# Kernel tuning notes

Hardware: AMD Instinct MI355X
Metric: run time of the kernel (lower is better)

## Reference

```python
import jax, jax.numpy as jnp
import numpy as np

SEQ_LEN = 2048
EMB_DIM = 1024
HIDDEN = 1024
VOCAB = 50257
OUT = 50257


def setup_inputs() -> dict:
    key = jax.random.key(0)
    ks = jax.random.split(key, 8)
    s = 0.02
    input_seq = jax.random.randint(ks[0], (SEQ_LEN,), 0, VOCAB)
    emb = jax.random.normal(ks[1], (VOCAB, EMB_DIM), dtype=jnp.float32) * s
    # PyTorch nn.LSTM params: weight_ih [4H, E], weight_hh [4H, H], biases [4H]
    W_ih = jax.random.normal(ks[2], (4 * HIDDEN, EMB_DIM), dtype=jnp.float32) * s
    W_hh = jax.random.normal(ks[3], (4 * HIDDEN, HIDDEN), dtype=jnp.float32) * s
    b_ih = jax.random.normal(ks[4], (4 * HIDDEN,), dtype=jnp.float32) * s
    b_hh = jax.random.normal(ks[5], (4 * HIDDEN,), dtype=jnp.float32) * s
    W_out = jax.random.normal(ks[6], (OUT, HIDDEN), dtype=jnp.float32) * s
    b_out = jax.random.normal(ks[7], (OUT,), dtype=jnp.float32) * s
    return {"input_seq": input_seq, "emb": emb, "W_ih": W_ih, "W_hh": W_hh,
            "b_ih": b_ih, "b_hh": b_hh, "W_out": W_out, "b_out": b_out}


def _lstm_forward(x, W_ih, W_hh, b_ih, b_hh):
    # x: [S, E]; batch dim (=1 in the torch module) is collapsed away.
    H = W_hh.shape[1]
    # Precompute input contribution to all gates for every timestep: [S, 4H]
    x_gates = x @ W_ih.T + (b_ih + b_hh)

    def step(carry, xg):
        h, c = carry
        g = xg + h @ W_hh.T  # [4H]
        i, f, gg, o = jnp.split(g, 4)  # PyTorch gate order: i, f, g, o
        i = jax.nn.sigmoid(i)
        f = jax.nn.sigmoid(f)
        gg = jnp.tanh(gg)
        o = jax.nn.sigmoid(o)
        c = f * c + i * gg
        h = o * jnp.tanh(c)
        return (h, c), h

    h0 = jnp.zeros((H,), dtype=x.dtype)
    c0 = jnp.zeros((H,), dtype=x.dtype)
    _, hs = jax.lax.scan(step, (h0, c0), x_gates)
    return hs  # [S, H]


def reference(input_seq, emb, W_ih, W_hh, b_ih, b_hh, W_out, b_out):
    x = emb[input_seq]  # [S, E] embedding lookup
    hs = _lstm_forward(x, W_ih, W_hh, b_ih, b_hh)  # [S, H]
    logits = hs @ W_out.T + b_out  # [S, OUT]
    return jax.nn.log_softmax(logits, axis=1)
```

## Files before the change

kernel.cpp:

```cpp
#include <hip/hip_runtime.h>
#include <hip/hip_bf16.h>

#define SEQ 2048
#define EMB 1024
#define HID 1024
#define G4  4096
#define VOC 50257
#define VPAD 50304
#define KDIM 1024

typedef short bhalf8 __attribute__((ext_vector_type(8)));
typedef float f32x4  __attribute__((ext_vector_type(4)));

typedef __attribute__((address_space(3))) void lds_void;
typedef __attribute__((address_space(1))) const void gbl_cvoid;

__device__ __forceinline__ void direct_lds16(void* lds, const void* g) {
    __builtin_amdgcn_global_load_lds((gbl_cvoid*)g, (lds_void*)lds, 16, 0, 0);
}

__device__ __forceinline__ unsigned short f2b(float f) {
    unsigned u = __float_as_uint(f);
    unsigned r = u + 0x7fffu + ((u >> 16) & 1u);
    return (unsigned short)(r >> 16);
}

__global__ void f32_to_bf16_k(const float* __restrict__ src, unsigned short* __restrict__ dst,
                              long n_src, long n_dst) {
    long i = ((long)blockIdx.x * 256 + threadIdx.x) * 4;
    if (i >= n_dst) return;
    unsigned short o0 = 0, o1 = 0, o2 = 0, o3 = 0;
    if (i < n_src) {
        f32x4 v = *(const f32x4*)&src[i];
        o0 = f2b(v[0]); o1 = f2b(v[1]); o2 = f2b(v[2]); o3 = f2b(v[3]);
    }
    ushort4 o; o.x = o0; o.y = o1; o.z = o2; o.w = o3;
    *(ushort4*)&dst[i] = o;
}

__global__ void embed_cvt_k(const int* __restrict__ seq, const float* __restrict__ emb,
                            unsigned short* __restrict__ xb) {
    int s = blockIdx.x;
    int k = threadIdx.x * 4;
    long row = (long)seq[s] * EMB;
    f32x4 v = *(const f32x4*)&emb[row + k];
    ushort4 o; o.x = f2b(v[0]); o.y = f2b(v[1]); o.z = f2b(v[2]); o.w = f2b(v[3]);
    *(ushort4*)&xb[(long)s * EMB + k] = o;
}

__global__ void bias_sum_k(const float* __restrict__ a, const float* __restrict__ b,
                           float* __restrict__ o) {
    int i = blockIdx.x * 256 + threadIdx.x;
    if (i < G4) o[i] = a[i] + b[i];
}

__global__ __launch_bounds__(256)
void gemm_bt_k(const unsigned short* __restrict__ A, const unsigned short* __restrict__ Bt,
               const float* __restrict__ bias, float* __restrict__ C,
               int M, int Nreal, int K, int ldc) {
    __shared__ unsigned short lA[128 * 64];
    __shared__ unsigned short lB[128 * 64];
    const int tid  = threadIdx.x;
    const int wave = tid >> 6;
    const int lane = tid & 63;
    const int m0 = blockIdx.x * 128;
    const int n0 = blockIdx.y * 128;
    const int wm = (wave >> 1) * 64;
    const int wn = (wave & 1) * 64;
    const int quad = lane >> 4, l16 = lane & 15;
    const int srow = lane >> 3;
    const int scol = (lane & 7) * 8;

    f32x4 acc[4][4] = {};

    for (int k0 = 0; k0 < K; k0 += 64) {
#pragma unroll
        for (int c = 0; c < 4; ++c) {
            int r0 = wave * 32 + c * 8;
            const unsigned short* ga = A  + (long)(m0 + r0 + srow) * K + k0 + scol;
            direct_lds16(&lA[r0 * 64], ga);
            const unsigned short* gb = Bt + (long)(n0 + r0 + srow) * K + k0 + scol;
            direct_lds16(&lB[r0 * 64], gb);
        }
        __syncthreads();
#pragma unroll
        for (int kk = 0; kk < 2; ++kk) {
            bhalf8 af[4], bf[4];
#pragma unroll
            for (int i = 0; i < 4; ++i) {
                af[i] = *(const bhalf8*)&lA[(wm + i * 16 + l16) * 64 + kk * 32 + quad * 8];
                bf[i] = *(const bhalf8*)&lB[(wn + i * 16 + l16) * 64 + kk * 32 + quad * 8];
            }
#pragma unroll
            for (int i = 0; i < 4; ++i)
#pragma unroll
                for (int j = 0; j < 4; ++j)
                    acc[i][j] = __builtin_amdgcn_mfma_f32_16x16x32_bf16(af[i], bf[j], acc[i][j], 0, 0, 0);
        }
        __syncthreads();
    }
#pragma unroll
    for (int i = 0; i < 4; ++i) {
        int gm = m0 + wm + i * 16 + quad * 4;
#pragma unroll
        for (int j = 0; j < 4; ++j) {
            int gn = n0 + wn + j * 16 + l16;
            if (gn < Nreal) {
                float bv = bias[gn];
#pragma unroll
                for (int r = 0; r < 4; ++r)
                    C[(long)(gm + r) * ldc + gn] = acc[i][j][r] + bv;
            }
        }
    }
}

__global__ __launch_bounds__(256) __attribute__((amdgpu_waves_per_eu(1, 1)))
void lstm_seq_k(const float* __restrict__ W_hh, const float* __restrict__ xg,
                unsigned short* __restrict__ hs_b, unsigned long long* __restrict__ hbuf) {
    const int tid  = threadIdx.x;
    const int wg   = blockIdx.x;
    const int wave = tid >> 6;
    const int lane = tid & 63;
    const int gate = lane >> 4;
    const int seg  = lane & 15;
    const int u    = wg * 4 + wave;
    const int grow = gate * HID + u;

    __shared__ __align__(16) float h_lds[2][HID];

    f32x4 w[16];
#pragma unroll
    for (int m = 0; m < 16; ++m)
        w[m] = *(const f32x4*)&W_hh[(long)grow * HID + (m * 16 + seg) * 4];

    const float sc = (gate == 2) ? 2.f : 1.f;
    const float sb = sc - 1.f;

#pragma unroll
    for (int q = 0; q < 4; ++q) h_lds[0][tid + q * 256] = 0.f;
    float c = 0.f;

    for (int t = 0; t < SEQ; ++t) {
        const int cur = t & 1;
        float xgv = (seg == 0) ? xg[(long)t * G4 + grow] : 0.f;
        if (t > 0) {
            const unsigned long long want = (unsigned long long)t;
            const unsigned long long* src = &hbuf[(1 - cur) * HID];
            const int e0 = tid, e1 = tid + 256, e2 = tid + 512, e3 = tid + 768;
            unsigned long long v0, v1, v2, v3;
            do {
                v0 = __hip_atomic_load(&src[e0], __ATOMIC_RELAXED, __HIP_MEMORY_SCOPE_AGENT);
                v1 = __hip_atomic_load(&src[e1], __ATOMIC_RELAXED, __HIP_MEMORY_SCOPE_AGENT);
                v2 = __hip_atomic_load(&src[e2], __ATOMIC_RELAXED, __HIP_MEMORY_SCOPE_AGENT);
                v3 = __hip_atomic_load(&src[e3], __ATOMIC_RELAXED, __HIP_MEMORY_SCOPE_AGENT);
            } while (((v0 >> 32) != want) | ((v1 >> 32) != want) |
                     ((v2 >> 32) != want) | ((v3 >> 32) != want));
            h_lds[cur][e0] = __uint_as_float((unsigned)v0);
            h_lds[cur][e1] = __uint_as_float((unsigned)v1);
            h_lds[cur][e2] = __uint_as_float((unsigned)v2);
            h_lds[cur][e3] = __uint_as_float((unsigned)v3);
        }
        __syncthreads();

        float a0 = 0.f, a1 = 0.f, a2 = 0.f, a3 = 0.f;
        const f32x4* h4 = (const f32x4*)&h_lds[cur][0];
#pragma unroll
        for (int m = 0; m < 16; ++m) {
            f32x4 hv = h4[m * 16 + seg];
            a0 += w[m][0] * hv[0];
            a1 += w[m][1] * hv[1];
            a2 += w[m][2] * hv[2];
            a3 += w[m][3] * hv[3];
        }
        float acc = (a0 + a1) + (a2 + a3);
        acc += __shfl_xor(acc, 8);
        acc += __shfl_xor(acc, 4);
        acc += __shfl_xor(acc, 2);
        acc += __shfl_xor(acc, 1);

        float a = 0.f;
        if (seg == 0) {
            float g = acc + xgv;
            float s = 1.f / (1.f + __expf(-sc * g));
            a = sc * s - sb;
        }
        float iv = __shfl(a, 0);
        float fv = __shfl(a, 16);
        float gv = __shfl(a, 32);
        float ov = __shfl(a, 48);
        if (lane == 0) {
            c = fv * c + iv * gv;
            float th = 2.f / (1.f + __expf(-2.f * c)) - 1.f;
            float h = ov * th;
            unsigned long long pk = ((unsigned long long)(t + 1) << 32)
                                  | (unsigned long long)__float_as_uint(h);
            __hip_atomic_store(&hbuf[cur * HID + u], pk, __ATOMIC_RELAXED, __HIP_MEMORY_SCOPE_AGENT);
            hs_b[(long)t * HID + u] = f2b(h);
        }
    }
}

__global__ __launch_bounds__(256)
void log_softmax_k(float* __restrict__ X) {
    const int tid = threadIdx.x;
    const long base = (long)blockIdx.x * VOC;
    float* p = X + base;
    const int head = (4 - (int)(base & 3)) & 3;
    const int n4 = (VOC - head) >> 2;
    const int tail_start = head + n4 * 4;
    f32x4* p4 = (f32x4*)(p + head);

    float m = -INFINITY, s = 0.f;
    auto upd = [&](float x) {
        float nm = fmaxf(m, x);
        s = s * __expf(m - nm) + __expf(x - nm);
        m = nm;
    };
    for (int i = tid; i < n4; i += 256) {
        f32x4 v = p4[i];
        upd(v[0]); upd(v[1]); upd(v[2]); upd(v[3]);
    }
    if (tid == 0) {
        for (int i = 0; i < head; ++i) upd(p[i]);
        for (int i = tail_start; i < VOC; ++i) upd(p[i]);
    }
#pragma unroll
    for (int o = 32; o; o >>= 1) {
        float m2 = __shfl_xor(m, o), s2 = __shfl_xor(s, o);
        float nm = fmaxf(m, m2);
        s = s * __expf(m - nm) + s2 * __expf(m2 - nm);
        m = nm;
    }
    __shared__ float sm[4], ss[4], sL;
    if ((tid & 63) == 0) { sm[tid >> 6] = m; ss[tid >> 6] = s; }
    __syncthreads();
    if (tid == 0) {
        m = sm[0]; s = ss[0];
        for (int wv = 1; wv < 4; ++wv) {
            float m2 = sm[wv], s2 = ss[wv];
            float nm = fmaxf(m, m2);
            s = s * __expf(m - nm) + s2 * __expf(m2 - nm);
            m = nm;
        }
        sL = m + __logf(s);
    }
    __syncthreads();
    const float L = sL;
    for (int i = tid; i < n4; i += 256) {
        f32x4 v = p4[i];
        v[0] -= L; v[1] -= L; v[2] -= L; v[3] -= L;
        p4[i] = v;
    }
    if (tid == 0) {
        for (int i = 0; i < head; ++i) p[i] -= L;
        for (int i = tail_start; i < VOC; ++i) p[i] -= L;
    }
}

extern "C" void kernel_launch(void* const* d_in, const int* in_sizes, int n_in,
                              void* d_out, int out_size, void* d_ws, size_t ws_size,
                              hipStream_t stream) {
    const int*   seq   = (const int*)d_in[0];
    const float* emb   = (const float*)d_in[1];
    const float* W_ih  = (const float*)d_in[2];
    const float* W_hh  = (const float*)d_in[3];
    const float* b_ih  = (const float*)d_in[4];
    const float* b_hh  = (const float*)d_in[5];
    const float* W_out = (const float*)d_in[6];
    const float* b_out = (const float*)d_in[7];
    float* out = (float*)d_out;

    size_t off = 0;
    auto carve = [&](size_t bytes) {
        void* p = (char*)d_ws + off;
        off += (bytes + 255) & ~(size_t)255;
        return p;
    };
    unsigned short* wWout = (unsigned short*)carve((size_t)VPAD * KDIM * 2);
    unsigned short* wWih  = (unsigned short*)carve((size_t)G4 * KDIM * 2);
    unsigned short* wX    = (unsigned short*)carve((size_t)SEQ * EMB * 2);
    unsigned short* wHs   = (unsigned short*)carve((size_t)SEQ * HID * 2);
    float*          wXg   = (float*)carve((size_t)SEQ * G4 * 4);
    float*          wBsum = (float*)carve((size_t)G4 * 4);
    unsigned long long* wHbuf = (unsigned long long*)carve((size_t)2 * HID * 8);

    f32_to_bf16_k<<<(int)(((size_t)VPAD * KDIM / 4 + 255) / 256), 256, 0, stream>>>(
        W_out, wWout, (long)VOC * KDIM, (long)VPAD * KDIM);
    f32_to_bf16_k<<<(int)(((size_t)G4 * KDIM / 4 + 255) / 256), 256, 0, stream>>>(
        W_ih, wWih, (long)G4 * KDIM, (long)G4 * KDIM);
    embed_cvt_k<<<SEQ, 256, 0, stream>>>(seq, emb, wX);
    bias_sum_k<<<(G4 + 255) / 256, 256, 0, stream>>>(b_ih, b_hh, wBsum);

    gemm_bt_k<<<dim3(SEQ / 128, G4 / 128), 256, 0, stream>>>(
        wX, wWih, wBsum, wXg, SEQ, G4, KDIM, G4);

    lstm_seq_k<<<256, 256, 0, stream>>>(W_hh, wXg, wHs, wHbuf);

    gemm_bt_k<<<dim3(SEQ / 128, VPAD / 128), 256, 0, stream>>>(
        wHs, wWout, b_out, out, SEQ, VOC, KDIM, VOC);

    log_softmax_k<<<SEQ, 256, 0, stream>>>(out);
}
```

Baseline: 7.894 ms.

## Replace tagged 64-bit h exchange with per-step zeroed stream and LSB flag

The cross-block hidden-state exchange used to write 64-bit (step tag, value) pairs into a double buffer, and each thread polled four separate 8-byte atomics. It now writes every step's h into its own slot of a zero-initialised [SEQ, HID] buffer, with the lowest mantissa bit forced to 1 as a ready flag. Each thread polls one 16-byte load that bypasses the caches. The next step's xg value is also prefetched after the barrier, taking that load off the critical path. The cost is an extra zeroing kernel, a larger workspace, and a one-ulp perturbation of h in the recurrence.

```diff
diff --git a/kernel.cpp b/kernel.cpp
--- a/kernel.cpp
+++ b/kernel.cpp
@@ -11,6 +11,7 @@
 
 typedef short bhalf8 __attribute__((ext_vector_type(8)));
 typedef float f32x4  __attribute__((ext_vector_type(4)));
+typedef unsigned u32x4 __attribute__((ext_vector_type(4)));
 
 typedef __attribute__((address_space(3))) void lds_void;
 typedef __attribute__((address_space(1))) const void gbl_cvoid;
@@ -36,6 +37,11 @@
     }
     ushort4 o; o.x = o0; o.y = o1; o.z = o2; o.w = o3;
     *(ushort4*)&dst[i] = o;
+}
+
+__global__ void zero_k(unsigned* __restrict__ p, long n4) {
+    long i = (long)blockIdx.x * 256 + threadIdx.x;
+    if (i < n4) ((u32x4*)p)[i] = (u32x4){0u, 0u, 0u, 0u};
 }
 
 __global__ void embed_cvt_k(const int* __restrict__ seq, const float* __restrict__ emb,
@@ -117,7 +123,7 @@
 
 __global__ __launch_bounds__(256) __attribute__((amdgpu_waves_per_eu(1, 1)))
 void lstm_seq_k(const float* __restrict__ W_hh, const float* __restrict__ xg,
-                unsigned short* __restrict__ hs_b, unsigned long long* __restrict__ hbuf) {
+                unsigned short* __restrict__ hs_b, unsigned* __restrict__ hstream) {
     const int tid  = threadIdx.x;
     const int wg   = blockIdx.x;
     const int wave = tid >> 6;
@@ -141,27 +147,25 @@
     for (int q = 0; q < 4; ++q) h_lds[0][tid + q * 256] = 0.f;
     float c = 0.f;
 
+    float xg_next = (seg == 0) ? xg[grow] : 0.f;
+
     for (int t = 0; t < SEQ; ++t) {
         const int cur = t & 1;
-        float xgv = (seg == 0) ? xg[(long)t * G4 + grow] : 0.f;
+        const float xgv = xg_next;
         if (t > 0) {
-            const unsigned long long want = (unsigned long long)t;
-            const unsigned long long* src = &hbuf[(1 - cur) * HID];
-            const int e0 = tid, e1 = tid + 256, e2 = tid + 512, e3 = tid + 768;
-            unsigned long long v0, v1, v2, v3;
+            const unsigned* src = &hstream[(long)(t - 1) * HID + 4 * tid];
+            u32x4 v;
             do {
-                v0 = __hip_atomic_load(&src[e0], __ATOMIC_RELAXED, __HIP_MEMORY_SCOPE_AGENT);
-                v1 = __hip_atomic_load(&src[e1], __ATOMIC_RELAXED, __HIP_MEMORY_SCOPE_AGENT);
-                v2 = __hip_atomic_load(&src[e2], __ATOMIC_RELAXED, __HIP_MEMORY_SCOPE_AGENT);
-                v3 = __hip_atomic_load(&src[e3], __ATOMIC_RELAXED, __HIP_MEMORY_SCOPE_AGENT);
-            } while (((v0 >> 32) != want) | ((v1 >> 32) != want) |
-                     ((v2 >> 32) != want) | ((v3 >> 32) != want));
-            h_lds[cur][e0] = __uint_as_float((unsigned)v0);
-            h_lds[cur][e1] = __uint_as_float((unsigned)v1);
-            h_lds[cur][e2] = __uint_as_float((unsigned)v2);
-            h_lds[cur][e3] = __uint_as_float((unsigned)v3);
+                asm volatile(
+                    "global_load_dwordx4 %0, %1, off sc0 sc1\n\t"
+                    "s_waitcnt vmcnt(0)"
+                    : "=&v"(v) : "v"(src) : "memory");
+            } while (((v[0] & v[1] & v[2] & v[3]) & 1u) == 0u);
+            ((u32x4*)&h_lds[cur][0])[tid] = v;
         }
         __syncthreads();
+
+        if (seg == 0 && t + 1 < SEQ) xg_next = xg[(long)(t + 1) * G4 + grow];
 
         float a0 = 0.f, a1 = 0.f, a2 = 0.f, a3 = 0.f;
         const f32x4* h4 = (const f32x4*)&h_lds[cur][0];
@@ -193,9 +197,10 @@
             c = fv * c + iv * gv;
             float th = 2.f / (1.f + __expf(-2.f * c)) - 1.f;
             float h = ov * th;
-            unsigned long long pk = ((unsigned long long)(t + 1) << 32)
-                                  | (unsigned long long)__float_as_uint(h);
-            __hip_atomic_store(&hbuf[cur * HID + u], pk, __ATOMIC_RELAXED, __HIP_MEMORY_SCOPE_AGENT);
+            unsigned pk = __float_as_uint(h) | 1u;
+            unsigned* dp = &hstream[(long)t * HID + u];
+            asm volatile("global_store_dword %0, %1, off sc0 sc1"
+                         :: "v"(dp), "v"(pk) : "memory");
             hs_b[(long)t * HID + u] = f2b(h);
         }
     }
@@ -283,7 +288,10 @@
     unsigned short* wHs   = (unsigned short*)carve((size_t)SEQ * HID * 2);
     float*          wXg   = (float*)carve((size_t)SEQ * G4 * 4);
     float*          wBsum = (float*)carve((size_t)G4 * 4);
-    unsigned long long* wHbuf = (unsigned long long*)carve((size_t)2 * HID * 8);
+    unsigned*       wHstream = (unsigned*)carve((size_t)SEQ * HID * 4);
+
+    zero_k<<<(int)(((size_t)SEQ * HID / 4 + 255) / 256), 256, 0, stream>>>(
+        wHstream, (long)SEQ * HID / 4);
 
     f32_to_bf16_k<<<(int)(((size_t)VPAD * KDIM / 4 + 255) / 256), 256, 0, stream>>>(
         W_out, wWout, (long)VOC * KDIM, (long)VPAD * KDIM);
@@ -295,7 +303,7 @@
     gemm_bt_k<<<dim3(SEQ / 128, G4 / 128), 256, 0, stream>>>(
         wX, wWih, wBsum, wXg, SEQ, G4, KDIM, G4);
 
-    lstm_seq_k<<<256, 256, 0, stream>>>(W_hh, wXg, wHs, wHbuf);
+    lstm_seq_k<<<256, 256, 0, stream>>>(W_hh, wXg, wHs, wHstream);
 
     gemm_bt_k<<<dim3(SEQ / 128, VPAD / 128), 256, 0, stream>>>(
         wHs, wWout, b_out, out, SEQ, VOC, KDIM, VOC);
```

Measured after the change: 6.450 ms. -18.3%, faster.
